# Kernel optimization log

Measured on AMD Instinct MI355X. Metric: run time of the kernel, lower is better.

The kernel has to match this reference:

```python
import jax, jax.numpy as jnp
import numpy as np

PI = float(np.pi)

def setup_inputs() -> dict:
    key = jax.random.key(0)
    # Pixel-like values in [0, 255)
    inputs = jax.random.uniform(key, (32768, 3, 32, 32), dtype=jnp.float32) * 255.0
    return {"inputs": inputs}

def reference(inputs) -> jnp.ndarray:
    B = inputs.shape[0]
    # 4x4 average pooling per channel, then channel mean -> [B, 8, 8]
    patches = inputs.reshape(B, 3, 8, 8, 4, 4).mean(axis=(-1, -2)).mean(axis=1)
    angles = patches.reshape(B, -1) / 255.0 * PI - PI / 2.0  # [B, 64]
    # RY(theta) on |0>, then <Z> = cos(theta) exactly (no entangling gates)
    return jnp.cos(angles)
```

## Files before the change

### kernel.cpp

```cpp
#include <hip/hip_runtime.h>

#define PI_F 3.14159265358979323846f

__global__ __launch_bounds__(768) void qa_pool_cos_kernel(
    const float4* __restrict__ in4, float* __restrict__ out)
{
    __shared__ float partial[192];

    int b   = blockIdx.x;
    int tid = threadIdx.x;

    float4 v = in4[(size_t)b * 768 + tid];
    float s = (v.x + v.y) + (v.z + v.w);

    s += __shfl_xor(s, 1, 64);
    s += __shfl_xor(s, 2, 64);

    if ((tid & 3) == 0) {
        int c = tid >> 8;
        int p = (tid & 255) >> 2;
        partial[c * 64 + p] = s;
    }
    __syncthreads();

    if (tid < 64) {
        float total = partial[tid] + partial[64 + tid] + partial[128 + tid];
        float ang   = total * (1.0f / 48.0f) * (PI_F / 255.0f) - (PI_F * 0.5f);
        out[(size_t)b * 64 + tid] = __cosf(ang);
    }
}

extern "C" void kernel_launch(void* const* d_in, const int* in_sizes, int n_in,
                              void* d_out, int out_size, void* d_ws, size_t ws_size,
                              hipStream_t stream) {
    const float4* in4 = (const float4*)d_in[0];
    float*        out = (float*)d_out;

    int B = out_size / 64;
    qa_pool_cos_kernel<<<B, 768, 0, stream>>>(in4, out);
}
```

Measured before the change: 502.7 us.

## Process four images per 256-thread block, summing channels in registers

```diff
diff --git a/kernel.cpp b/kernel.cpp
--- a/kernel.cpp
+++ b/kernel.cpp
@@ -2,31 +2,38 @@
 
 #define PI_F 3.14159265358979323846f
 
-__global__ __launch_bounds__(768) void qa_pool_cos_kernel(
+__global__ __launch_bounds__(256) void qa_pool_cos_kernel(
     const float4* __restrict__ in4, float* __restrict__ out)
 {
-    __shared__ float partial[192];
+    int tid = threadIdx.x;
+    size_t b0   = (size_t)blockIdx.x * 4;
+    size_t base = b0 * 768;
 
-    int b   = blockIdx.x;
-    int tid = threadIdx.x;
+    float s[4];
+#pragma unroll
+    for (int j = 0; j < 4; ++j) {
+        size_t bb = base + (size_t)j * 768;
+        float4 v0 = in4[bb + tid];
+        float4 v1 = in4[bb + 256 + tid];
+        float4 v2 = in4[bb + 512 + tid];
+        s[j] = ((v0.x + v0.y) + (v0.z + v0.w))
+             + ((v1.x + v1.y) + (v1.z + v1.w))
+             + ((v2.x + v2.y) + (v2.z + v2.w));
+    }
 
-    float4 v = in4[(size_t)b * 768 + tid];
-    float s = (v.x + v.y) + (v.z + v.w);
-
-    s += __shfl_xor(s, 1, 64);
-    s += __shfl_xor(s, 2, 64);
+#pragma unroll
+    for (int j = 0; j < 4; ++j) {
+        s[j] += __shfl_xor(s[j], 1, 64);
+        s[j] += __shfl_xor(s[j], 2, 64);
+    }
 
     if ((tid & 3) == 0) {
-        int c = tid >> 8;
-        int p = (tid & 255) >> 2;
-        partial[c * 64 + p] = s;
-    }
-    __syncthreads();
-
-    if (tid < 64) {
-        float total = partial[tid] + partial[64 + tid] + partial[128 + tid];
-        float ang   = total * (1.0f / 48.0f) * (PI_F / 255.0f) - (PI_F * 0.5f);
-        out[(size_t)b * 64 + tid] = __cosf(ang);
+        int p = tid >> 2;
+#pragma unroll
+        for (int j = 0; j < 4; ++j) {
+            float ang = s[j] * (1.0f / 48.0f) * (PI_F / 255.0f) - (PI_F * 0.5f);
+            out[(b0 + j) * 64 + p] = __cosf(ang);
+        }
     }
 }
 
@@ -36,6 +43,7 @@
     const float4* in4 = (const float4*)d_in[0];
     float*        out = (float*)d_out;
 
-    int B = out_size / 64;
-    qa_pool_cos_kernel<<<B, 768, 0, stream>>>(in4, out);
+    int B    = out_size / 64;
+    int grid = B / 4;
+    qa_pool_cos_kernel<<<grid, 256, 0, stream>>>(in4, out);
 }
```

After: 512.3 us. No clear change (+1.9%).
